# Kernel tuning notes

Hardware: AMD Instinct MI355X
Metric: run time of the kernel (lower is better)

Reference implementation:

```python
import jax, jax.numpy as jnp
import numpy as np

B, S, D = 4, 2048, 1024
H, HD = 16, 64  # n_heads, head_dim (n_kv_heads == n_heads -> n_rep = 1)
WINDOW = 256
ROPE_THETA = 10000.0


def setup_inputs() -> dict:
    key = jax.random.key(0)
    ks = jax.random.split(key, 5)
    x = jax.random.normal(ks[0], (B, S, D), dtype=jnp.float32)
    scale = 0.02
    wq = jax.random.normal(ks[1], (D, D), dtype=jnp.float32) * scale
    wk = jax.random.normal(ks[2], (D, D), dtype=jnp.float32) * scale
    wv = jax.random.normal(ks[3], (D, D), dtype=jnp.float32) * scale
    wo = jax.random.normal(ks[4], (D, D), dtype=jnp.float32) * scale
    # RoPE frequencies: freqs_cis[t, i] = exp(1j * t / theta^(2i/HD)), i in [0, HD/2)
    inv_freq = 1.0 / (ROPE_THETA ** (jnp.arange(0, HD, 2, dtype=jnp.float32) / HD))
    t = jnp.arange(S, dtype=jnp.float32)
    ang = t[:, None] * inv_freq[None, :]  # [S, HD/2]
    return {"x": x, "freqs_cos": jnp.cos(ang), "freqs_sin": jnp.sin(ang),
            "wq": wq, "wk": wk, "wv": wv, "wo": wo}


def _apply_rope(xq, xk, cos, sin):
    # xq/xk: [B, S, H, HD]; cos/sin: [S, HD/2] broadcast as [1, S, 1, HD/2]
    def rot(v):
        vr = v.reshape(*v.shape[:-1], HD // 2, 2)
        v0, v1 = vr[..., 0], vr[..., 1]
        c = cos[None, :, None, :]
        s = sin[None, :, None, :]
        o0 = v0 * c - v1 * s
        o1 = v0 * s + v1 * c
        return jnp.stack([o0, o1], axis=-1).reshape(v.shape)
    return rot(xq), rot(xk)


def reference(x, freqs_cos, freqs_sin, wq, wk, wv, wo):
    b, s, _ = x.shape
    xq = (x @ wq.T).reshape(b, s, H, HD)
    xk = (x @ wk.T).reshape(b, s, H, HD)
    xv = (x @ wv.T).reshape(b, s, H, HD)
    xq, xk = _apply_rope(xq, xk, freqs_cos, freqs_sin)
    # [B, H, S, S] scores
    scores = jnp.einsum('bqhd,bkhd->bhqk', xq, xk) / jnp.sqrt(jnp.float32(HD))
    pos = jnp.arange(s)
    # masked (disallowed) when j > i (future) or i - j >= window
    bad = (pos[None, :] > pos[:, None]) | (pos[:, None] - pos[None, :] >= WINDOW)
    scores = jnp.where(bad[None, None], -jnp.inf, scores)
    attn = jax.nn.softmax(scores.astype(jnp.float32), axis=-1).astype(xq.dtype)
    out = jnp.einsum('bhqk,bkhd->bqhd', attn, xv).reshape(b, s, H * HD)
    return out @ wo.T
```

## Files before the change

kernel.cpp:

```cpp
#include <hip/hip_runtime.h>
#include <hip/hip_bf16.h>


typedef __bf16 bf16_t;
typedef __attribute__((ext_vector_type(8))) __bf16 bf16x8;
typedef __attribute__((ext_vector_type(4))) __bf16 bf16x4;
typedef __attribute__((ext_vector_type(4))) float f32x4;

#define MFMA16(a, b, c) __builtin_amdgcn_mfma_f32_16x16x32_bf16((a), (b), (c), 0, 0, 0)

__device__ __forceinline__ void async16(const void* g, void* l) {
    __builtin_amdgcn_global_load_lds(
        (const __attribute__((address_space(1))) unsigned int*)g,
        (__attribute__((address_space(3))) unsigned int*)l, 16, 0, 0);
}

#define BAR() do { asm volatile("" ::: "memory"); __builtin_amdgcn_s_barrier(); \
                   asm volatile("" ::: "memory"); } while (0)
#define VMC(N) asm volatile("s_waitcnt vmcnt(" #N ")" ::: "memory")
#define LGKM0() asm volatile("s_waitcnt lgkmcnt(0)" ::: "memory")

#define CBS 131072L

__global__ __launch_bounds__(256) void cvt_all(const float* __restrict__ x,
                                               const float* __restrict__ wq,
                                               const float* __restrict__ wk,
                                               const float* __restrict__ wv,
                                               const float* __restrict__ wo,
                                               bf16_t* __restrict__ xbf,
                                               bf16_t* __restrict__ wqkv,
                                               bf16_t* __restrict__ wobf) {
    const int blk = blockIdx.x;
    const float* s;
    bf16_t* d;
    int base;
    if (blk < 4096)      { s = x;  d = xbf;            base = blk; }
    else if (blk < 4608) { s = wq; d = wqkv;           base = blk - 4096; }
    else if (blk < 5120) { s = wk; d = wqkv + 1048576; base = blk - 4608; }
    else if (blk < 5632) { s = wv; d = wqkv + 2097152; base = blk - 5120; }
    else                 { s = wo; d = wobf;           base = blk - 5632; }
    const int i = (base * 256 + threadIdx.x) * 8;
    float4 a = *(const float4*)(s + i);
    float4 b = *(const float4*)(s + i + 4);
    bf16x8 o;
    o[0] = (bf16_t)a.x; o[1] = (bf16_t)a.y; o[2] = (bf16_t)a.z; o[3] = (bf16_t)a.w;
    o[4] = (bf16_t)b.x; o[5] = (bf16_t)b.y; o[6] = (bf16_t)b.z; o[7] = (bf16_t)b.w;
    *(bf16x8*)(d + i) = o;
}

__global__ __launch_bounds__(512, 1) __attribute__((amdgpu_waves_per_eu(2)))
void gemm192_qkv(const bf16_t* __restrict__ A, const bf16_t* __restrict__ Bw,
                 const float* __restrict__ fcos, const float* __restrict__ fsin,
                 bf16_t* __restrict__ Qo, bf16_t* __restrict__ Ko,
                 bf16_t* __restrict__ VT, int M, int N, int K) {
    __shared__ __attribute__((aligned(16))) bf16_t As[32768];
    __shared__ __attribute__((aligned(16))) bf16_t Bs[24576];
    const int tid = threadIdx.x;
    const int l = tid & 63, w = tid >> 6;
    const int lr = l & 15, lg = l >> 4;
    const int wr = w >> 2, wc = w & 3;

    const int nwg = gridDim.x * gridDim.y;
    const int flat = blockIdx.y * gridDim.x + blockIdx.x;
    const int swz = (flat & 7) * (nwg >> 3) + (flat >> 3);
    const int bx = swz % gridDim.x, by = swz / gridDim.x;
    const long m0 = (long)by * 256, n0 = (long)bx * 192;
    const int NT = K >> 6;
    const int NI = NT >> 1;

    const int p  = w * 1024 + l * 16;
    const int pp = p ^ (((p >> 9) & 1) << 5);
    const int st = pp >> 10;
    const int rSt = (st >> 1) * 16 + ((pp >> 6) & 15);
    const int cSt = (st & 1) * 32 + ((pp >> 4) & 3) * 8;
    const bf16_t* aS = A  + (m0 + rSt) * K + cSt;
    const bf16_t* bS = Bw + (n0 + rSt) * K + cSt;
    const long uK = 64L * K;

    auto stageA = [&](int b, int u, int t) {
        async16(aS + (long)u * uK + (long)t * 64,
                (char*)As + b * 32768 + u * 8192 + w * 1024);
    };
    auto stageB = [&](int b, int u, int t) {
        async16(bS + (long)u * uK + (long)t * 64,
                (char*)Bs + b * 24576 + u * 8192 + w * 1024);
    };

    f32x4 acc[8][3] = {};
    bf16x8 afX[4], afY[4], bfX[3], bfY[3];
    const int swd = (lr & 8) << 2;

    auto loadAF = [&](int b, int mh, int ks, bf16x8 (&dst)[4]) {
#pragma unroll
        for (int mi = 0; mi < 4; ++mi) {
            const int off = (wr * 2 + mh) * 8192 + (mi * 2 + ks) * 1024 +
                            lr * 64 + lg * 16;
            dst[mi] = *(const bf16x8*)((const char*)As + b * 32768 + (off ^ swd));
        }
    };
    auto loadBF = [&](int b, int ks, bf16x8 (&dst)[3]) {
#pragma unroll
        for (int nj = 0; nj < 3; ++nj) {
            const int rg = wc * 48 + nj * 16 + lr;
            const int off = (rg >> 6) * 8192 + (((rg >> 4) & 3) * 2 + ks) * 1024 +
                            lr * 64 + lg * 16;
            dst[nj] = *(const bf16x8*)((const char*)Bs + b * 24576 + (off ^ swd));
        }
    };

#define QMM(MH, AF, BF) do {                                                   \
    __builtin_amdgcn_s_setprio(1);                                             \
    _Pragma("unroll")                                                          \
    for (int mi = 0; mi < 4; ++mi)                                             \
        _Pragma("unroll")                                                      \
        for (int nj = 0; nj < 3; ++nj)                                         \
            acc[(MH)*4+mi][nj] = MFMA16((AF)[mi], (BF)[nj], acc[(MH)*4+mi][nj]); \
    __builtin_amdgcn_s_setprio(0);                                             \
} while (0)

    stageA(0, 0, 0); stageA(0, 1, 0); stageA(0, 2, 0); stageA(0, 3, 0);
    stageB(0, 0, 0); stageB(0, 1, 0); stageB(0, 2, 0);
    stageB(1, 0, 1); stageB(1, 1, 1); stageB(1, 2, 1);
    VMC(3);
    BAR();

#pragma unroll 1
    for (int it = 0; it < NI - 1; ++it) {
        const int T = 2 * it;
        loadAF(0, 0, 0, afX); loadBF(0, 0, bfX);
        stageA(1, 0, T + 1); stageA(1, 1, T + 1);
        BAR(); QMM(0, afX, bfX); BAR();
        loadAF(0, 1, 0, afY);
        stageA(1, 2, T + 1); stageA(1, 3, T + 1);
        BAR(); QMM(1, afY, bfX); BAR();
        loadAF(0, 0, 1, afX); loadBF(0, 1, bfY);
        BAR(); QMM(0, afX, bfY); BAR();
        loadAF(0, 1, 1, afY);
        stageB(0, 0, T + 2);
        BAR(); QMM(1, afY, bfY); VMC(1); BAR();
        loadAF(1, 0, 0, afX); loadBF(1, 0, bfX);
        stageB(0, 1, T + 2); stageB(0, 2, T + 2);
        BAR(); QMM(0, afX, bfX); BAR();
        loadAF(1, 1, 0, afY);
        stageA(0, 0, T + 2); stageA(0, 1, T + 2);
        BAR(); QMM(1, afY, bfX); BAR();
        loadAF(1, 0, 1, afX); loadBF(1, 1, bfY);
        stageA(0, 2, T + 2); stageA(0, 3, T + 2);
        BAR(); QMM(0, afX, bfY); BAR();
        loadAF(1, 1, 1, afY);
        stageB(1, 0, T + 3); stageB(1, 1, T + 3); stageB(1, 2, T + 3);
        BAR(); QMM(1, afY, bfY); VMC(3); BAR();
    }

    {
        loadAF(0, 0, 0, afX); loadBF(0, 0, bfX);
        stageA(1, 0, NT - 1); stageA(1, 1, NT - 1);
        BAR(); QMM(0, afX, bfX); BAR();
        loadAF(0, 1, 0, afY);
        stageA(1, 2, NT - 1); stageA(1, 3, NT - 1);
        BAR(); QMM(1, afY, bfX); BAR();
        loadAF(0, 0, 1, afX); loadBF(0, 1, bfY);
        BAR(); QMM(0, afX, bfY); BAR();
        loadAF(0, 1, 1, afY);
        BAR(); QMM(1, afY, bfY);
        VMC(0); BAR();
        loadAF(1, 0, 0, afX); loadBF(1, 0, bfX);
        QMM(0, afX, bfX);
        loadAF(1, 1, 0, afY);
        QMM(1, afY, bfX);
        loadAF(1, 0, 1, afX); loadBF(1, 1, bfY);
        QMM(0, afX, bfY);
        loadAF(1, 1, 1, afY);
        QMM(1, afY, bfY);
    }
#undef QMM

    bf16_t* scr = (w < 6) ? (bf16_t*)((char*)As + w * 5120)
                          : (bf16_t*)((char*)Bs + (w - 6) * 5120);
    asm volatile("" ::: "memory");

    const int tl = l & 31, cg = l >> 5;
    const int chb = cg * 8;

#pragma unroll
    for (int nj = 0; nj < 3; ++nj) {
        const int cbase = (int)n0 + wc * 48 + nj * 16;
        const int cls = cbase >> 10;

#pragma unroll
        for (int ai = 0; ai < 8; ++ai)
#pragma unroll
            for (int j = 0; j < 4; ++j)
                scr[(ai * 16 + lg * 4 + j) * 20 + lr] = (bf16_t)acc[ai][nj][j];
        LGKM0();
        asm volatile("" ::: "memory");

        if (cls == 2) {
            const int ch = l >> 2;
            const int sub = l & 3;
            const int d16 = cbase - 2048 + ch;
            const int hh = d16 >> 6, dd = d16 & 63;
            const long T0 = m0 + wr * 128;
            const int bb = (int)(T0 >> 11);
            const int s0 = (int)(T0 & 2047);
            bf16_t* vrow = VT + ((long)((bb * 16 + hh) * 64 + dd) * 2048) + s0;
#pragma unroll
            for (int qq = 0; qq < 4; ++qq) {
                const int tb8 = qq * 32 + sub * 8;
                bf16x8 o;
#pragma unroll
                for (int j = 0; j < 8; ++j) {
                    const int f = ((j & 3) << 1) | (j >> 2);
                    o[j] = scr[(tb8 + f) * 20 + ch];
                }
                *(bf16x8*)(vrow + tb8) = o;
            }
        } else {
            const int cq = cbase & 1023;
            const float sc = (cls == 0) ? 0.125f : 1.f;
            bf16_t* qk = ((cls == 0) ? Qo : Ko) + (long)(cq >> 4) * CBS + chb;
            const int p2b = ((cbase & 63) >> 1) + cg * 4;
#pragma unroll
            for (int qq = 0; qq < 4; ++qq) {
                const int t = tl + qq * 32;
                bf16x4 vlo = *(const bf16x4*)&scr[t * 20 + chb];
                bf16x4 vhi = *(const bf16x4*)&scr[t * 20 + chb + 4];
                const long gt = m0 + wr * 128 + t;
                const int s0 = (int)(gt & 2047);
                const float4 cc = *(const float4*)(fcos + s0 * 32 + p2b);
                const float4 sn = *(const float4*)(fsin + s0 * 32 + p2b);
                bf16x8 o;
                float e0, e1;
                e0 = (float)vlo[0]; e1 = (float)vlo[1];
                o[0] = (bf16_t)((e0 * cc.x - e1 * sn.x) * sc);
                o[1] = (bf16_t)((e0 * sn.x + e1 * cc.x) * sc);
                e0 = (float)vlo[2]; e1 = (float)vlo[3];
                o[2] = (bf16_t)((e0 * cc.y - e1 * sn.y) * sc);
                o[3] = (bf16_t)((e0 * sn.y + e1 * cc.y) * sc);
                e0 = (float)vhi[0]; e1 = (float)vhi[1];
                o[4] = (bf16_t)((e0 * cc.z - e1 * sn.z) * sc);
                o[5] = (bf16_t)((e0 * sn.z + e1 * cc.z) * sc);
                e0 = (float)vhi[2]; e1 = (float)vhi[3];
                o[6] = (bf16_t)((e0 * cc.w - e1 * sn.w) * sc);
                o[7] = (bf16_t)((e0 * sn.w + e1 * cc.w) * sc);
                *(bf16x8*)(qk + gt * 16) = o;
            }
        }
        LGKM0();
        asm volatile("" ::: "memory");
    }
}

template <typename OUT>
__global__ __launch_bounds__(512, 2) void gemm256(const bf16_t* __restrict__ A,
                                                  const bf16_t* __restrict__ Bw,
                                                  OUT* __restrict__ C,
                                                  int M, int N, int K) {
    __shared__ __attribute__((aligned(16))) bf16_t As[49152];
    __shared__ __attribute__((aligned(16))) bf16_t Bs[24576];
    const int tid = threadIdx.x;
    const int l = tid & 63, w = tid >> 6;
    const int lr = l & 15, lg = l >> 4;
    const int wr = w >> 1, wc = w & 1;

    const int nwg = gridDim.x * gridDim.y;
    const int flat = blockIdx.y * gridDim.x + blockIdx.x;
    const int swz = (flat & 7) * (nwg >> 3) + (flat >> 3);
    const int bx = swz % gridDim.x, by = swz / gridDim.x;
    const long m0 = (long)by * 256, n0 = (long)bx * 128;
    const int NT = K >> 6;

    int rS[2], cS[2];
#pragma unroll
    for (int i = 0; i < 2; ++i) {
        const int p  = i * 8192 + w * 1024 + l * 16;
        const int pp = p ^ (((p >> 9) & 1) << 5);
        const int st = pp >> 10;
        rS[i] = (st >> 1) * 16 + ((pp >> 6) & 15);
        cS[i] = (st & 1) * 32 + ((pp >> 4) & 3) * 8;
    }
    const bf16_t* aSrc0 = A  + (m0 + rS[0]) * K + cS[0];
    const bf16_t* aSrc1 = A  + (m0 + rS[1]) * K + cS[1];
    const bf16_t* bSrc0 = Bw + (n0 + rS[0]) * K + cS[0];
    const bf16_t* bSrc1 = Bw + (n0 + rS[1]) * K + cS[1];
    const long hK = 128L * K;

    auto stageA = [&](int b, int h, int t) {
        char* d = (char*)As + b * 32768 + h * 16384 + w * 1024;
        const long o = (long)h * hK + (long)t * 64;
        async16(aSrc0 + o, d);
        async16(aSrc1 + o, d + 8192);
    };
    auto stageB = [&](int b, int t) {
        char* d = (char*)Bs + b * 16384 + w * 1024;
        const long o = (long)t * 64;
        async16(bSrc0 + o, d);
        async16(bSrc1 + o, d + 8192);
    };

    f32x4 acc[4][4] = {};
    bf16x8 af[4][2], blo[2][2], bhi[2][2];
    const int swd = (lr & 8) << 2;

    auto loadA = [&](int b) {
#pragma unroll
        for (int mi = 0; mi < 4; ++mi)
#pragma unroll
            for (int ks = 0; ks < 2; ++ks) {
                const int ra = (wr & 1) * 64 + mi * 16 + lr;
                const int off = ((ra >> 4) * 2 + ks) * 1024 + (ra & 15) * 64 + lg * 16;
                af[mi][ks] = *(const bf16x8*)((const char*)As + b * 32768 +
                                              (wr >> 1) * 16384 + (off ^ swd));
            }
    };
    auto loadB = [&](int b, int nh, bf16x8 (&dst)[2][2]) {
#pragma unroll
        for (int nj = 0; nj < 2; ++nj)
#pragma unroll
            for (int ks = 0; ks < 2; ++ks) {
                const int rb = wc * 64 + (nh * 2 + nj) * 16 + lr;
                const int off = ((rb >> 4) * 2 + ks) * 1024 + (rb & 15) * 64 + lg * 16;
                dst[nj][ks] = *(const bf16x8*)((const char*)Bs + b * 16384 +
                                               (off ^ swd));
            }
    };

#define QMM(NH, BF) do {                                                       \
    __builtin_amdgcn_s_setprio(1);                                             \
    _Pragma("unroll")                                                          \
    for (int mi = 0; mi < 4; ++mi) {                                           \
        acc[mi][(NH)*2]   = MFMA16(af[mi][0], (BF)[0][0], acc[mi][(NH)*2]);    \
        acc[mi][(NH)*2]   = MFMA16(af[mi][1], (BF)[0][1], acc[mi][(NH)*2]);    \
        acc[mi][(NH)*2+1] = MFMA16(af[mi][0], (BF)[1][0], acc[mi][(NH)*2+1]);  \
        acc[mi][(NH)*2+1] = MFMA16(af[mi][1], (BF)[1][1], acc[mi][(NH)*2+1]);  \
    }                                                                          \
    __builtin_amdgcn_s_setprio(0);                                             \
} while (0)

    stageA(0, 0, 0); stageA(0, 1, 0); stageB(0, 0);
    stageA(1, 0, 1); stageA(1, 1, 1); stageB(1, 1);
    VMC(6);
    BAR();

    int bc = 0;
#pragma unroll 1
    for (int t = 0; t < NT - 2; ++t) {
        const int bn = (bc + 2 >= 3) ? bc - 1 : bc + 2;
        loadA(bc); loadB(bc, 0, blo); stageA(bn, 0, t + 2); stageA(bn, 1, t + 2);
        BAR(); QMM(0, blo); BAR();
        loadB(bc, 1, bhi); stageB(bn, t + 2);
        BAR(); QMM(1, bhi);
        if (t < NT - 3) { VMC(6); } else { VMC(0); }
        BAR();
        bc = (bc + 1 >= 3) ? 0 : bc + 1;
    }
    {
        loadA(bc); loadB(bc, 0, blo);
        QMM(0, blo);
        loadB(bc, 1, bhi);
        QMM(1, bhi);
        const int b2 = (bc + 1 >= 3) ? 0 : bc + 1;
        loadA(b2); loadB(b2, 0, blo);
        QMM(0, blo);
        loadB(b2, 1, bhi);
        QMM(1, bhi);
    }
#undef QMM

#pragma unroll
    for (int mi = 0; mi < 4; ++mi)
#pragma unroll
        for (int ni = 0; ni < 4; ++ni)
#pragma unroll
            for (int j = 0; j < 4; ++j) {
                long r = m0 + wr * 64 + mi * 16 + lg * 4 + j;
                long c = n0 + wc * 64 + ni * 16 + lr;
                C[r * N + c] = (OUT)acc[mi][ni][j];
            }
}

__global__ __launch_bounds__(256, 4) void attn_win4(const bf16_t* __restrict__ Q,
                                                    const bf16_t* __restrict__ Kb,
                                                    const bf16_t* __restrict__ VT,
                                                    bf16_t* __restrict__ Ao) {
    __shared__ __attribute__((aligned(16))) bf16_t kld[2 * 4096];
    __shared__ __attribute__((aligned(16))) bf16_t vld[2 * 4096];
    const int raw = blockIdx.x;
    const int mswz = ((raw & 7) << 8) | (raw >> 3);
    const int qt = mswz & 31, bh = mswz >> 5;
    const int h = bh & 15, b = bh >> 4;
    const int l = threadIdx.x & 63, w = threadIdx.x >> 6;
    const int lr = l & 15, lg = l >> 4;
    const int q0 = qt * 64 + w * 16;
    const int q = q0 + lr;
    const int tb = qt - 4;

    const bf16_t* Qh = Q  + (long)(4 * h) * CBS + (long)(b * 2048) * 16;
    const bf16_t* Kh = Kb + (long)(4 * h) * CBS + (long)(b * 2048) * 16;
    const bf16_t* Vp = VT + (long)bh * 64 * 2048;

    auto stageT = [&](int u, int bs) {
        const int kt = tb + u;
        const int kt64 = (kt < 0 ? 0 : kt) * 64;
#pragma unroll
        for (int part = 0; part < 2; ++part) {
            const int seg = w * 2 + part;
            const int r = seg * 8 + (l >> 3);
            const int sc = (l & 7) ^ ((r >> 1) & 7);
            async16(Kh + (sc >> 1) * CBS + (long)(kt64 + r) * 16 + (sc & 1) * 8,
                    (char*)kld + bs * 8192 + seg * 1024);
            async16(Vp + (long)r * 2048 + kt64 + sc * 8,
                    (char*)vld + bs * 8192 + seg * 1024);
        }
    };

    stageT(0, 0);
    const bf16x8 qb0 = *(const bf16x8*)&Qh[(lg >> 1) * CBS + (long)q * 16 + (lg & 1) * 8];
    const bf16x8 qb1 = *(const bf16x8*)&Qh[(2 + (lg >> 1)) * CBS + (long)q * 16 + (lg & 1) * 8];
    VMC(0);
    BAR();

    float mrun = -1000.f, lsum = 0.f;
    f32x4 o0 = {0.f, 0.f, 0.f, 0.f}, o1 = {0.f, 0.f, 0.f, 0.f};
    f32x4 o2 = {0.f, 0.f, 0.f, 0.f}, o3 = {0.f, 0.f, 0.f, 0.f};
    const int swv = (lr >> 1) & 7;

    const char* kbase;
    const char* vbase;
    int k0s;

#define QKCORE(HH, MM)                                                           \
        const int row_ = (HH) * 32 + 2 * lr + (MM);                              \
        const int sw_ = (row_ >> 1) & 7;                                         \
        bf16x8 k0_ = *(const bf16x8*)(kbase + row_ * 128 + ((lg ^ sw_) << 4));   \
        bf16x8 k1_ = *(const bf16x8*)(kbase + row_ * 128 + (((4 + lg) ^ sw_) << 4)); \
        f32x4 s_ = {0.f, 0.f, 0.f, 0.f};                                         \
        s_ = MFMA16(k0_, qb0, s_);                                               \
        s_ = MFMA16(k1_, qb1, s_);

#define QKF_F(DST, HH, MM)                                                       \
    f32x4 DST; { QKCORE(HH, MM)                                                  \
        const int kb_ = k0s + (HH) * 32 + (MM) + lg * 8;                         \
        DST[0] = ((kb_ >= 0) & ((unsigned)(q - kb_) < 256u))         ? s_[0] : -1e30f; \
        DST[1] = ((kb_ + 2 >= 0) & ((unsigned)(q - kb_ - 2) < 256u)) ? s_[1] : -1e30f; \
        DST[2] = ((kb_ + 4 >= 0) & ((unsigned)(q - kb_ - 4) < 256u)) ? s_[2] : -1e30f; \
        DST[3] = ((kb_ + 6 >= 0) & ((unsigned)(q - kb_ - 6) < 256u)) ? s_[3] : -1e30f; \
    }

#define QKF_U(DST, HH, MM)                                                       \
    f32x4 DST; { QKCORE(HH, MM)                                                  \
        const int d_ = q - (k0s + (HH) * 32 + (MM) + lg * 8);                    \
        DST[0] = (d_ < 256)     ? s_[0] : -1e30f;                                \
        DST[1] = (d_ - 2 < 256) ? s_[1] : -1e30f;                                \
        DST[2] = (d_ - 4 < 256) ? s_[2] : -1e30f;                                \
        DST[3] = (d_ - 6 < 256) ? s_[3] : -1e30f;                                \
    }

#define QKF_L(DST, HH, MM)                                                       \
    f32x4 DST; { QKCORE(HH, MM)                                                  \
        const int d_ = q - (k0s + (HH) * 32 + (MM) + lg * 8);                    \
        DST[0] = (d_ >= 0)     ? s_[0] : -1e30f;                                 \
        DST[1] = (d_ - 2 >= 0) ? s_[1] : -1e30f;                                 \
        DST[2] = (d_ - 4 >= 0) ? s_[2] : -1e30f;                                 \
        DST[3] = (d_ - 6 >= 0) ? s_[3] : -1e30f;                                 \
    }

#define QKF_N(DST, HH, MM)                                                       \
    f32x4 DST; { QKCORE(HH, MM)                                                  \
        DST[0] = s_[0]; DST[1] = s_[1]; DST[2] = s_[2]; DST[3] = s_[3];          \
    }

#define EXV(S_) {                                                                \
        S_[0] = __expf(S_[0] - mnew); S_[1] = __expf(S_[1] - mnew);              \
        S_[2] = __expf(S_[2] - mnew); S_[3] = __expf(S_[3] - mnew);              \
        rs += (S_[0] + S_[1]) + (S_[2] + S_[3]); }

#define PVF(NT, HH, PB) {                                                        \
        bf16x8 va_ = *(const bf16x8*)(vbase + ((NT) * 16 + lr) * 128 +           \
                                      ((((HH) * 4 + lg) ^ swv) << 4));           \
        o##NT = MFMA16(va_, PB, o##NT); }

#define TILEBODY(QKM) {                                                          \
        QKM(sA, 0, 0) QKM(sB, 0, 1) QKM(sC, 1, 0) QKM(sD, 1, 1)                  \
        float tm = fmaxf(fmaxf(fmaxf(sA[0], sA[1]), fmaxf(sA[2], sA[3])),        \
                         fmaxf(fmaxf(sB[0], sB[1]), fmaxf(sB[2], sB[3])));       \
        tm = fmaxf(tm, fmaxf(fmaxf(fmaxf(sC[0], sC[1]), fmaxf(sC[2], sC[3])),    \
                             fmaxf(fmaxf(sD[0], sD[1]), fmaxf(sD[2], sD[3]))));  \
        tm = fmaxf(tm, __shfl_xor(tm, 16));                                      \
        tm = fmaxf(tm, __shfl_xor(tm, 32));                                      \
        const float mnew = fmaxf(mrun, tm);                                      \
        const float alpha = __expf(mrun - mnew);                                 \
        mrun = mnew;                                                             \
        float rs = 0.f;                                                          \
        EXV(sA) EXV(sB) EXV(sC) EXV(sD)                                          \
        rs += __shfl_xor(rs, 16);                                                \
        rs += __shfl_xor(rs, 32);                                                \
        lsum = lsum * alpha + rs;                                                \
        o0[0] *= alpha; o0[1] *= alpha; o0[2] *= alpha; o0[3] *= alpha;          \
        o1[0] *= alpha; o1[1] *= alpha; o1[2] *= alpha; o1[3] *= alpha;          \
        o2[0] *= alpha; o2[1] *= alpha; o2[2] *= alpha; o2[3] *= alpha;          \
        o3[0] *= alpha; o3[1] *= alpha; o3[2] *= alpha; o3[3] *= alpha;          \
        bf16x8 pb0, pb1;                                                         \
        pb0[0] = (bf16_t)sA[0]; pb0[1] = (bf16_t)sA[1]; pb0[2] = (bf16_t)sA[2]; pb0[3] = (bf16_t)sA[3]; \
        pb0[4] = (bf16_t)sB[0]; pb0[5] = (bf16_t)sB[1]; pb0[6] = (bf16_t)sB[2]; pb0[7] = (bf16_t)sB[3]; \
        pb1[0] = (bf16_t)sC[0]; pb1[1] = (bf16_t)sC[1]; pb1[2] = (bf16_t)sC[2]; pb1[3] = (bf16_t)sC[3]; \
        pb1[4] = (bf16_t)sD[0]; pb1[5] = (bf16_t)sD[1]; pb1[6] = (bf16_t)sD[2]; pb1[7] = (bf16_t)sD[3]; \
        PVF(0, 0, pb0) PVF(1, 0, pb0) PVF(2, 0, pb0) PVF(3, 0, pb0)              \
        PVF(0, 1, pb1) PVF(1, 1, pb1) PVF(2, 1, pb1) PVF(3, 1, pb1)              \
    }

#define ITER(U, QKM) {                                                           \
        if ((U) < 4) stageT((U) + 1, ((U) + 1) & 1);                             \
        kbase = (const char*)kld + ((U) & 1) * 8192;                             \
        vbase = (const char*)vld + ((U) & 1) * 8192;                             \
        k0s = (tb + (U)) * 64;                                                   \
        TILEBODY(QKM)                                                            \
        if ((U) < 4) { VMC(0); BAR(); }                                          \
    }

    if (qt >= 4) {
        ITER(0, QKF_U)
        ITER(1, QKF_N)
        ITER(2, QKF_N)
        ITER(3, QKF_N)
        ITER(4, QKF_L)
    } else {
        ITER(0, QKF_F)
        ITER(1, QKF_F)
        ITER(2, QKF_F)
        ITER(3, QKF_F)
        ITER(4, QKF_F)
    }
#undef ITER
#undef TILEBODY
#undef QKF_F
#undef QKF_U
#undef QKF_L
#undef QKF_N
#undef QKCORE
#undef EXV
#undef PVF

    const float rinv = 1.0f / lsum;
    bf16_t* aor = Ao + ((long)(b * 2048) + q) * 1024 + h * 64;
#define EPI(NT, OA_) {                                                           \
        bf16x4 ov_;                                                             \
        ov_[0] = (bf16_t)(OA_[0] * rinv); ov_[1] = (bf16_t)(OA_[1] * rinv);      \
        ov_[2] = (bf16_t)(OA_[2] * rinv); ov_[3] = (bf16_t)(OA_[3] * rinv);      \
        *(bf16x4*)(aor + (NT) * 16 + lg * 4) = ov_; }
    EPI(0, o0) EPI(1, o1) EPI(2, o2) EPI(3, o3)
#undef EPI
}

extern "C" void kernel_launch(void* const* d_in, const int* in_sizes, int n_in,
                              void* d_out, int out_size, void* d_ws, size_t ws_size,
                              hipStream_t stream) {
    (void)in_sizes; (void)n_in; (void)out_size; (void)ws_size;
    const float* x    = (const float*)d_in[0];
    const float* fcos = (const float*)d_in[1];
    const float* fsin = (const float*)d_in[2];
    const float* wq   = (const float*)d_in[3];
    const float* wk   = (const float*)d_in[4];
    const float* wv   = (const float*)d_in[5];
    const float* wo   = (const float*)d_in[6];
    float* out = (float*)d_out;

    char* ws = (char*)d_ws;
    bf16_t* xbf   = (bf16_t*)(ws);
    bf16_t* wqkv  = (bf16_t*)(ws + 16777216);
    bf16_t* wobf  = (bf16_t*)(ws + 23068672);
    bf16_t* qbuf  = (bf16_t*)(ws + 41943040);
    bf16_t* kbuf  = (bf16_t*)(ws + 75497472);
    bf16_t* vtb   = (bf16_t*)(ws + 92274688);
    bf16_t* aob   = xbf;

    cvt_all<<<6144, 256, 0, stream>>>(x, wq, wk, wv, wo, xbf, wqkv, wobf);

    gemm192_qkv<<<dim3(16, 32), 512, 0, stream>>>(xbf, wqkv, fcos, fsin,
                                                  qbuf, kbuf, vtb,
                                                  8192, 3072, 1024);
    attn_win4<<<2048, 256, 0, stream>>>(qbuf, kbuf, vtb, aob);
    gemm256<float><<<dim3(8, 32), 512, 0, stream>>>(aob, wobf, out, 8192, 1024, 1024);
}
```

Baseline: 120.6 us.

## Widen QKV GEMM tile from 256x192 to 256x256 with restructured pipeline

The QKV projection GEMM now uses 256x256 output tiles instead of 256x192, so the grid shrinks from 16x32 to 12x32 workgroups. Each wave now computes a 128x64 block with 8x4 accumulators. Staging and fragment loads are reorganised into half-tiles with a new barrier and wait schedule. The goal is higher arithmetic intensity and less redundant A-operand traffic. The cost is more registers, more LDS, and 384 workgroups, which is fewer than the 512 before and may leave the GPU's CUs less evenly loaded.

```diff
diff --git a/kernel.cpp b/kernel.cpp
--- a/kernel.cpp
+++ b/kernel.cpp
@@ -49,12 +49,12 @@
 }
 
 __global__ __launch_bounds__(512, 1) __attribute__((amdgpu_waves_per_eu(2)))
-void gemm192_qkv(const bf16_t* __restrict__ A, const bf16_t* __restrict__ Bw,
+void gemm256_qkv(const bf16_t* __restrict__ A, const bf16_t* __restrict__ Bw,
                  const float* __restrict__ fcos, const float* __restrict__ fsin,
                  bf16_t* __restrict__ Qo, bf16_t* __restrict__ Ko,
                  bf16_t* __restrict__ VT, int M, int N, int K) {
     __shared__ __attribute__((aligned(16))) bf16_t As[32768];
-    __shared__ __attribute__((aligned(16))) bf16_t Bs[24576];
+    __shared__ __attribute__((aligned(16))) bf16_t Bs[32768];
     const int tid = threadIdx.x;
     const int l = tid & 63, w = tid >> 6;
     const int lr = l & 15, lg = l >> 4;
@@ -64,114 +64,118 @@
     const int flat = blockIdx.y * gridDim.x + blockIdx.x;
     const int swz = (flat & 7) * (nwg >> 3) + (flat >> 3);
     const int bx = swz % gridDim.x, by = swz / gridDim.x;
-    const long m0 = (long)by * 256, n0 = (long)bx * 192;
+    const long m0 = (long)by * 256, n0 = (long)bx * 256;
     const int NT = K >> 6;
     const int NI = NT >> 1;
 
-    const int p  = w * 1024 + l * 16;
-    const int pp = p ^ (((p >> 9) & 1) << 5);
-    const int st = pp >> 10;
-    const int rSt = (st >> 1) * 16 + ((pp >> 6) & 15);
-    const int cSt = (st & 1) * 32 + ((pp >> 4) & 3) * 8;
-    const bf16_t* aS = A  + (m0 + rSt) * K + cSt;
-    const bf16_t* bS = Bw + (n0 + rSt) * K + cSt;
-    const long uK = 64L * K;
-
-    auto stageA = [&](int b, int u, int t) {
-        async16(aS + (long)u * uK + (long)t * 64,
-                (char*)As + b * 32768 + u * 8192 + w * 1024);
-    };
-    auto stageB = [&](int b, int u, int t) {
-        async16(bS + (long)u * uK + (long)t * 64,
-                (char*)Bs + b * 24576 + u * 8192 + w * 1024);
-    };
-
-    f32x4 acc[8][3] = {};
-    bf16x8 afX[4], afY[4], bfX[3], bfY[3];
+    int rS[2], cS[2];
+#pragma unroll
+    for (int i = 0; i < 2; ++i) {
+        const int p  = i * 8192 + w * 1024 + l * 16;
+        const int pp = p ^ (((p >> 9) & 1) << 5);
+        const int st = pp >> 10;
+        rS[i] = (st >> 1) * 16 + ((pp >> 6) & 15);
+        cS[i] = (st & 1) * 32 + ((pp >> 4) & 3) * 8;
+    }
+    const bf16_t* aSrc0 = A  + (m0 + rS[0]) * K + cS[0];
+    const bf16_t* aSrc1 = A  + (m0 + rS[1]) * K + cS[1];
+    const bf16_t* bSrc0 = Bw + (n0 + rS[0]) * K + cS[0];
+    const bf16_t* bSrc1 = Bw + (n0 + rS[1]) * K + cS[1];
+    const long hK = 128L * K;
+
+    auto stageA = [&](int b, int h, int t) {
+        char* d = (char*)As + b * 32768 + h * 16384 + w * 1024;
+        const long o = (long)h * hK + (long)t * 64;
+        async16(aSrc0 + o, d);
+        async16(aSrc1 + o, d + 8192);
+    };
+    auto stageB = [&](int b, int h, int t) {
+        char* d = (char*)Bs + b * 32768 + h * 16384 + w * 1024;
+        const long o = (long)h * hK + (long)t * 64;
+        async16(bSrc0 + o, d);
+        async16(bSrc1 + o, d + 8192);
+    };
+
+    f32x4 acc[8][4] = {};
+    bf16x8 af[4][2], bh0[2][2], bh1[2][2];
     const int swd = (lr & 8) << 2;
 
-    auto loadAF = [&](int b, int mh, int ks, bf16x8 (&dst)[4]) {
-#pragma unroll
-        for (int mi = 0; mi < 4; ++mi) {
-            const int off = (wr * 2 + mh) * 8192 + (mi * 2 + ks) * 1024 +
-                            lr * 64 + lg * 16;
-            dst[mi] = *(const bf16x8*)((const char*)As + b * 32768 + (off ^ swd));
-        }
-    };
-    auto loadBF = [&](int b, int ks, bf16x8 (&dst)[3]) {
-#pragma unroll
-        for (int nj = 0; nj < 3; ++nj) {
-            const int rg = wc * 48 + nj * 16 + lr;
-            const int off = (rg >> 6) * 8192 + (((rg >> 4) & 3) * 2 + ks) * 1024 +
-                            lr * 64 + lg * 16;
-            dst[nj] = *(const bf16x8*)((const char*)Bs + b * 24576 + (off ^ swd));
-        }
-    };
-
-#define QMM(MH, AF, BF) do {                                                   \
-    __builtin_amdgcn_s_setprio(1);                                             \
-    _Pragma("unroll")                                                          \
-    for (int mi = 0; mi < 4; ++mi)                                             \
-        _Pragma("unroll")                                                      \
-        for (int nj = 0; nj < 3; ++nj)                                         \
-            acc[(MH)*4+mi][nj] = MFMA16((AF)[mi], (BF)[nj], acc[(MH)*4+mi][nj]); \
-    __builtin_amdgcn_s_setprio(0);                                             \
+    auto loadA = [&](int b, int mh) {
+#pragma unroll
+        for (int i = 0; i < 4; ++i)
+#pragma unroll
+            for (int ks = 0; ks < 2; ++ks) {
+                const int off = ((mh * 4 + i) * 2 + ks) * 1024 + lr * 64 + lg * 16;
+                af[i][ks] = *(const bf16x8*)((const char*)As + b * 32768 +
+                                             wr * 16384 + (off ^ swd));
+            }
+    };
+    auto loadB = [&](int b, int nh, bf16x8 (&dst)[2][2]) {
+#pragma unroll
+        for (int j = 0; j < 2; ++j)
+#pragma unroll
+            for (int ks = 0; ks < 2; ++ks) {
+                const int off = (((wc & 1) * 4 + nh * 2 + j) * 2 + ks) * 1024 +
+                                lr * 64 + lg * 16;
+                dst[j][ks] = *(const bf16x8*)((const char*)Bs + b * 32768 +
+                                              (wc >> 1) * 16384 + (off ^ swd));
+            }
+    };
+
+#define QMM(MH, NH, BF) do {                                                        \
+    __builtin_amdgcn_s_setprio(1);                                                  \
+    _Pragma("unroll")                                                               \
+    for (int qi = 0; qi < 4; ++qi) {                                                \
+        acc[(MH)*4+qi][(NH)*2]   = MFMA16(af[qi][0], (BF)[0][0], acc[(MH)*4+qi][(NH)*2]);   \
+        acc[(MH)*4+qi][(NH)*2]   = MFMA16(af[qi][1], (BF)[0][1], acc[(MH)*4+qi][(NH)*2]);   \
+        acc[(MH)*4+qi][(NH)*2+1] = MFMA16(af[qi][0], (BF)[1][0], acc[(MH)*4+qi][(NH)*2+1]); \
+        acc[(MH)*4+qi][(NH)*2+1] = MFMA16(af[qi][1], (BF)[1][1], acc[(MH)*4+qi][(NH)*2+1]); \
+    }                                                                               \
+    __builtin_amdgcn_s_setprio(0);                                                  \
 } while (0)
 
-    stageA(0, 0, 0); stageA(0, 1, 0); stageA(0, 2, 0); stageA(0, 3, 0);
-    stageB(0, 0, 0); stageB(0, 1, 0); stageB(0, 2, 0);
-    stageB(1, 0, 1); stageB(1, 1, 1); stageB(1, 2, 1);
-    VMC(3);
+    stageB(0, 0, 0); stageB(0, 1, 0); stageA(0, 0, 0); stageA(0, 1, 0);
+    stageB(1, 0, 1); stageB(1, 1, 1);
+    VMC(4);
     BAR();
 
 #pragma unroll 1
     for (int it = 0; it < NI - 1; ++it) {
-        const int T = 2 * it;
-        loadAF(0, 0, 0, afX); loadBF(0, 0, bfX);
-        stageA(1, 0, T + 1); stageA(1, 1, T + 1);
-        BAR(); QMM(0, afX, bfX); BAR();
-        loadAF(0, 1, 0, afY);
-        stageA(1, 2, T + 1); stageA(1, 3, T + 1);
-        BAR(); QMM(1, afY, bfX); BAR();
-        loadAF(0, 0, 1, afX); loadBF(0, 1, bfY);
-        BAR(); QMM(0, afX, bfY); BAR();
-        loadAF(0, 1, 1, afY);
-        stageB(0, 0, T + 2);
-        BAR(); QMM(1, afY, bfY); VMC(1); BAR();
-        loadAF(1, 0, 0, afX); loadBF(1, 0, bfX);
-        stageB(0, 1, T + 2); stageB(0, 2, T + 2);
-        BAR(); QMM(0, afX, bfX); BAR();
-        loadAF(1, 1, 0, afY);
-        stageA(0, 0, T + 2); stageA(0, 1, T + 2);
-        BAR(); QMM(1, afY, bfX); BAR();
-        loadAF(1, 0, 1, afX); loadBF(1, 1, bfY);
-        stageA(0, 2, T + 2); stageA(0, 3, T + 2);
-        BAR(); QMM(0, afX, bfY); BAR();
-        loadAF(1, 1, 1, afY);
-        stageB(1, 0, T + 3); stageB(1, 1, T + 3); stageB(1, 2, T + 3);
-        BAR(); QMM(1, afY, bfY); VMC(3); BAR();
+        const int T = it * 2;
+        loadA(0, 0); loadB(0, 0, bh0); stageA(1, 0, T + 1);
+        BAR(); QMM(0, 0, bh0); BAR();
+        loadB(0, 1, bh1); stageA(1, 1, T + 1);
+        BAR(); QMM(0, 1, bh1); BAR();
+        loadA(0, 1); stageB(0, 0, T + 2);
+        BAR(); QMM(1, 0, bh0); BAR();
+        stageB(0, 1, T + 2);
+        BAR(); QMM(1, 1, bh1); VMC(4); BAR();
+        loadA(1, 0); loadB(1, 0, bh0); stageA(0, 0, T + 2);
+        BAR(); QMM(0, 0, bh0); BAR();
+        loadB(1, 1, bh1); stageA(0, 1, T + 2);
+        BAR(); QMM(0, 1, bh1); BAR();
+        loadA(1, 1); stageB(1, 0, T + 3);
+        BAR(); QMM(1, 0, bh0); BAR();
+        stageB(1, 1, T + 3);
+        BAR(); QMM(1, 1, bh1); VMC(4); BAR();
     }
 
     {
-        loadAF(0, 0, 0, afX); loadBF(0, 0, bfX);
-        stageA(1, 0, NT - 1); stageA(1, 1, NT - 1);
-        BAR(); QMM(0, afX, bfX); BAR();
-        loadAF(0, 1, 0, afY);
-        stageA(1, 2, NT - 1); stageA(1, 3, NT - 1);
-        BAR(); QMM(1, afY, bfX); BAR();
-        loadAF(0, 0, 1, afX); loadBF(0, 1, bfY);
-        BAR(); QMM(0, afX, bfY); BAR();
-        loadAF(0, 1, 1, afY);
-        BAR(); QMM(1, afY, bfY);
+        const int T = NT - 2;
+        loadA(0, 0); loadB(0, 0, bh0); stageA(1, 0, T + 1);
+        BAR(); QMM(0, 0, bh0); BAR();
+        loadB(0, 1, bh1); stageA(1, 1, T + 1);
+        BAR(); QMM(0, 1, bh1); BAR();
+        loadA(0, 1);
+        BAR(); QMM(1, 0, bh0); QMM(1, 1, bh1);
         VMC(0); BAR();
-        loadAF(1, 0, 0, afX); loadBF(1, 0, bfX);
-        QMM(0, afX, bfX);
-        loadAF(1, 1, 0, afY);
-        QMM(1, afY, bfX);
-        loadAF(1, 0, 1, afX); loadBF(1, 1, bfY);
-        QMM(0, afX, bfY);
-        loadAF(1, 1, 1, afY);
-        QMM(1, afY, bfY);
+        loadA(1, 0); loadB(1, 0, bh0);
+        QMM(0, 0, bh0);
+        loadB(1, 1, bh1);
+        QMM(0, 1, bh1);
+        loadA(1, 1);
+        QMM(1, 0, bh0);
+        QMM(1, 1, bh1);
     }
 #undef QMM
 
@@ -183,15 +187,15 @@
     const int chb = cg * 8;
 
 #pragma unroll
-    for (int nj = 0; nj < 3; ++nj) {
-        const int cbase = (int)n0 + wc * 48 + nj * 16;
+    for (int ni = 0; ni < 4; ++ni) {
+        const int cbase = (int)n0 + wc * 64 + ni * 16;
         const int cls = cbase >> 10;
 
 #pragma unroll
         for (int ai = 0; ai < 8; ++ai)
 #pragma unroll
             for (int j = 0; j < 4; ++j)
-                scr[(ai * 16 + lg * 4 + j) * 20 + lr] = (bf16_t)acc[ai][nj][j];
+                scr[(ai * 16 + lg * 4 + j) * 20 + lr] = (bf16_t)acc[ai][ni][j];
         LGKM0();
         asm volatile("" ::: "memory");
 
@@ -576,7 +580,7 @@
 
     cvt_all<<<6144, 256, 0, stream>>>(x, wq, wk, wv, wo, xbf, wqkv, wobf);
 
-    gemm192_qkv<<<dim3(16, 32), 512, 0, stream>>>(xbf, wqkv, fcos, fsin,
+    gemm256_qkv<<<dim3(12, 32), 512, 0, stream>>>(xbf, wqkv, fcos, fsin,
                                                   qbuf, kbuf, vtb,
                                                   8192, 3072, 1024);
     attn_win4<<<2048, 256, 0, stream>>>(qbuf, kbuf, vtb, aob);
```

New measurement: 138.1 us. +14.5%, slower.

## Restructure output-projection GEMM with double-buffered LDS and 2x4 wave layout

Applied to the files above, without the earlier changes.

Replaces the triple-buffered output projection GEMM with a double-buffered version that uses less LDS. The 8 waves are rearranged into a 2x4 grid, each computing 128x32, and loads and MFMAs are interleaved at finer granularity with per-quarter staging and barriers. The aim is to raise occupancy (waves_per_eu 2) and overlap global-to-LDS copies with compute better. In exchange it adds more barriers and has a shallower prefetch depth, which may expose memory latency.

```diff
diff --git a/kernel.cpp b/kernel.cpp
--- a/kernel.cpp
+++ b/kernel.cpp
@@ -251,17 +251,15 @@
     }
 }
 
-template <typename OUT>
-__global__ __launch_bounds__(512, 2) void gemm256(const bf16_t* __restrict__ A,
-                                                  const bf16_t* __restrict__ Bw,
-                                                  OUT* __restrict__ C,
-                                                  int M, int N, int K) {
-    __shared__ __attribute__((aligned(16))) bf16_t As[49152];
-    __shared__ __attribute__((aligned(16))) bf16_t Bs[24576];
+__global__ __launch_bounds__(512, 1) __attribute__((amdgpu_waves_per_eu(2)))
+void gemm128_o(const bf16_t* __restrict__ A, const bf16_t* __restrict__ Bw,
+               float* __restrict__ C, int M, int N, int K) {
+    __shared__ __attribute__((aligned(16))) bf16_t As[32768];
+    __shared__ __attribute__((aligned(16))) bf16_t Bs[16384];
     const int tid = threadIdx.x;
     const int l = tid & 63, w = tid >> 6;
     const int lr = l & 15, lg = l >> 4;
-    const int wr = w >> 1, wc = w & 1;
+    const int wr = w >> 2, wc = w & 3;
 
     const int nwg = gridDim.x * gridDim.y;
     const int flat = blockIdx.y * gridDim.x + blockIdx.x;
@@ -269,113 +267,123 @@
     const int bx = swz % gridDim.x, by = swz / gridDim.x;
     const long m0 = (long)by * 256, n0 = (long)bx * 128;
     const int NT = K >> 6;
-
-    int rS[2], cS[2];
-#pragma unroll
-    for (int i = 0; i < 2; ++i) {
-        const int p  = i * 8192 + w * 1024 + l * 16;
-        const int pp = p ^ (((p >> 9) & 1) << 5);
-        const int st = pp >> 10;
-        rS[i] = (st >> 1) * 16 + ((pp >> 6) & 15);
-        cS[i] = (st & 1) * 32 + ((pp >> 4) & 3) * 8;
-    }
-    const bf16_t* aSrc0 = A  + (m0 + rS[0]) * K + cS[0];
-    const bf16_t* aSrc1 = A  + (m0 + rS[1]) * K + cS[1];
-    const bf16_t* bSrc0 = Bw + (n0 + rS[0]) * K + cS[0];
-    const bf16_t* bSrc1 = Bw + (n0 + rS[1]) * K + cS[1];
-    const long hK = 128L * K;
-
-    auto stageA = [&](int b, int h, int t) {
-        char* d = (char*)As + b * 32768 + h * 16384 + w * 1024;
-        const long o = (long)h * hK + (long)t * 64;
-        async16(aSrc0 + o, d);
-        async16(aSrc1 + o, d + 8192);
-    };
-    auto stageB = [&](int b, int t) {
-        char* d = (char*)Bs + b * 16384 + w * 1024;
-        const long o = (long)t * 64;
-        async16(bSrc0 + o, d);
-        async16(bSrc1 + o, d + 8192);
-    };
-
-    f32x4 acc[4][4] = {};
-    bf16x8 af[4][2], blo[2][2], bhi[2][2];
+    const int NI = NT >> 1;
+
+    const int p  = w * 1024 + l * 16;
+    const int pp = p ^ (((p >> 9) & 1) << 5);
+    const int st = pp >> 10;
+    const int rSt = (st >> 1) * 16 + ((pp >> 6) & 15);
+    const int cSt = (st & 1) * 32 + ((pp >> 4) & 3) * 8;
+    const bf16_t* aS = A  + (m0 + rSt) * K + cSt;
+    const bf16_t* bS = Bw + (n0 + rSt) * K + cSt;
+    const long uK = 64L * K;
+
+    auto stageA = [&](int b, int u, int t) {
+        async16(aS + (long)u * uK + (long)t * 64,
+                (char*)As + b * 32768 + u * 8192 + w * 1024);
+    };
+    auto stageB = [&](int b, int u, int t) {
+        async16(bS + (long)u * uK + (long)t * 64,
+                (char*)Bs + b * 16384 + u * 8192 + w * 1024);
+    };
+
+    f32x4 acc[8][2] = {};
+    bf16x8 afX[4], afY[4], bfX[2], bfY[2];
     const int swd = (lr & 8) << 2;
 
-    auto loadA = [&](int b) {
-#pragma unroll
-        for (int mi = 0; mi < 4; ++mi)
-#pragma unroll
-            for (int ks = 0; ks < 2; ++ks) {
-                const int ra = (wr & 1) * 64 + mi * 16 + lr;
-                const int off = ((ra >> 4) * 2 + ks) * 1024 + (ra & 15) * 64 + lg * 16;
-                af[mi][ks] = *(const bf16x8*)((const char*)As + b * 32768 +
-                                              (wr >> 1) * 16384 + (off ^ swd));
-            }
-    };
-    auto loadB = [&](int b, int nh, bf16x8 (&dst)[2][2]) {
-#pragma unroll
-        for (int nj = 0; nj < 2; ++nj)
-#pragma unroll
-            for (int ks = 0; ks < 2; ++ks) {
-                const int rb = wc * 64 + (nh * 2 + nj) * 16 + lr;
-                const int off = ((rb >> 4) * 2 + ks) * 1024 + (rb & 15) * 64 + lg * 16;
-                dst[nj][ks] = *(const bf16x8*)((const char*)Bs + b * 16384 +
-                                               (off ^ swd));
-            }
-    };
-
-#define QMM(NH, BF) do {                                                       \
+    auto loadAF = [&](int b, int mh, int ks, bf16x8 (&dst)[4]) {
+#pragma unroll
+        for (int mi = 0; mi < 4; ++mi) {
+            const int off = (wr * 2 + mh) * 8192 + (mi * 2 + ks) * 1024 +
+                            lr * 64 + lg * 16;
+            dst[mi] = *(const bf16x8*)((const char*)As + b * 32768 + (off ^ swd));
+        }
+    };
+    auto loadBF = [&](int b, int ks, bf16x8 (&dst)[2]) {
+#pragma unroll
+        for (int nj = 0; nj < 2; ++nj) {
+            const int rg = wc * 32 + nj * 16 + lr;
+            const int off = (rg >> 6) * 8192 + (((rg >> 4) & 3) * 2 + ks) * 1024 +
+                            lr * 64 + lg * 16;
+            dst[nj] = *(const bf16x8*)((const char*)Bs + b * 16384 + (off ^ swd));
+        }
+    };
+
+#define QMM(MH, AF, BF) do {                                                   \
     __builtin_amdgcn_s_setprio(1);                                             \
     _Pragma("unroll")                                                          \
-    for (int mi = 0; mi < 4; ++mi) {                                           \
-        acc[mi][(NH)*2]   = MFMA16(af[mi][0], (BF)[0][0], acc[mi][(NH)*2]);    \
-        acc[mi][(NH)*2]   = MFMA16(af[mi][1], (BF)[0][1], acc[mi][(NH)*2]);    \
-        acc[mi][(NH)*2+1] = MFMA16(af[mi][0], (BF)[1][0], acc[mi][(NH)*2+1]);  \
-        acc[mi][(NH)*2+1] = MFMA16(af[mi][1], (BF)[1][1], acc[mi][(NH)*2+1]);  \
-    }                                                                          \
+    for (int mi = 0; mi < 4; ++mi)                                             \
+        _Pragma("unroll")                                                      \
+        for (int nj = 0; nj < 2; ++nj)                                         \
+            acc[(MH)*4+mi][nj] = MFMA16((AF)[mi], (BF)[nj], acc[(MH)*4+mi][nj]); \
     __builtin_amdgcn_s_setprio(0);                                             \
 } while (0)
 
-    stageA(0, 0, 0); stageA(0, 1, 0); stageB(0, 0);
-    stageA(1, 0, 1); stageA(1, 1, 1); stageB(1, 1);
-    VMC(6);
+    stageA(0, 0, 0); stageA(0, 1, 0); stageA(0, 2, 0); stageA(0, 3, 0);
+    stageB(0, 0, 0); stageB(0, 1, 0);
+    stageB(1, 0, 1); stageB(1, 1, 1);
+    VMC(2);
     BAR();
 
-    int bc = 0;
 #pragma unroll 1
-    for (int t = 0; t < NT - 2; ++t) {
-        const int bn = (bc + 2 >= 3) ? bc - 1 : bc + 2;
-        loadA(bc); loadB(bc, 0, blo); stageA(bn, 0, t + 2); stageA(bn, 1, t + 2);
-        BAR(); QMM(0, blo); BAR();
-        loadB(bc, 1, bhi); stageB(bn, t + 2);
-        BAR(); QMM(1, bhi);
-        if (t < NT - 3) { VMC(6); } else { VMC(0); }
-        BAR();
-        bc = (bc + 1 >= 3) ? 0 : bc + 1;
-    }
+    for (int it = 0; it < NI - 1; ++it) {
+        const int T = 2 * it;
+        loadAF(0, 0, 0, afX); loadBF(0, 0, bfX);
+        stageA(1, 0, T + 1); stageA(1, 1, T + 1);
+        BAR(); QMM(0, afX, bfX); BAR();
+        loadAF(0, 1, 0, afY);
+        stageA(1, 2, T + 1); stageA(1, 3, T + 1);
+        BAR(); QMM(1, afY, bfX); BAR();
+        loadAF(0, 0, 1, afX); loadBF(0, 1, bfY);
+        BAR(); QMM(0, afX, bfY); BAR();
+        loadAF(0, 1, 1, afY);
+        stageB(0, 0, T + 2); stageB(0, 1, T + 2);
+        BAR(); QMM(1, afY, bfY); VMC(2); BAR();
+        loadAF(1, 0, 0, afX); loadBF(1, 0, bfX);
+        stageA(0, 0, T + 2); stageA(0, 1, T + 2);
+        BAR(); QMM(0, afX, bfX); BAR();
+        loadAF(1, 1, 0, afY);
+        stageA(0, 2, T + 2); stageA(0, 3, T + 2);
+        BAR(); QMM(1, afY, bfX); BAR();
+        loadAF(1, 0, 1, afX); loadBF(1, 1, bfY);
+        BAR(); QMM(0, afX, bfY); BAR();
+        loadAF(1, 1, 1, afY);
+        stageB(1, 0, T + 3); stageB(1, 1, T + 3);
+        BAR(); QMM(1, afY, bfY); VMC(2); BAR();
+    }
+
     {
-        loadA(bc); loadB(bc, 0, blo);
-        QMM(0, blo);
-        loadB(bc, 1, bhi);
-        QMM(1, bhi);
-        const int b2 = (bc + 1 >= 3) ? 0 : bc + 1;
-        loadA(b2); loadB(b2, 0, blo);
-        QMM(0, blo);
-        loadB(b2, 1, bhi);
-        QMM(1, bhi);
+        loadAF(0, 0, 0, afX); loadBF(0, 0, bfX);
+        stageA(1, 0, NT - 1); stageA(1, 1, NT - 1);
+        BAR(); QMM(0, afX, bfX); BAR();
+        loadAF(0, 1, 0, afY);
+        stageA(1, 2, NT - 1); stageA(1, 3, NT - 1);
+        BAR(); QMM(1, afY, bfX); BAR();
+        loadAF(0, 0, 1, afX); loadBF(0, 1, bfY);
+        BAR(); QMM(0, afX, bfY); BAR();
+        loadAF(0, 1, 1, afY);
+        BAR(); QMM(1, afY, bfY);
+        VMC(0); BAR();
+        loadAF(1, 0, 0, afX); loadBF(1, 0, bfX);
+        QMM(0, afX, bfX);
+        loadAF(1, 1, 0, afY);
+        QMM(1, afY, bfX);
+        loadAF(1, 0, 1, afX); loadBF(1, 1, bfY);
+        QMM(0, afX, bfY);
+        loadAF(1, 1, 1, afY);
+        QMM(1, afY, bfY);
     }
 #undef QMM
 
 #pragma unroll
-    for (int mi = 0; mi < 4; ++mi)
-#pragma unroll
-        for (int ni = 0; ni < 4; ++ni)
+    for (int ai = 0; ai < 8; ++ai)
+#pragma unroll
+        for (int nj = 0; nj < 2; ++nj)
 #pragma unroll
             for (int j = 0; j < 4; ++j) {
-                long r = m0 + wr * 64 + mi * 16 + lg * 4 + j;
-                long c = n0 + wc * 64 + ni * 16 + lr;
-                C[r * N + c] = (OUT)acc[mi][ni][j];
+                long r = m0 + wr * 128 + ai * 16 + lg * 4 + j;
+                long c = n0 + wc * 32 + nj * 16 + lr;
+                C[r * (long)N + c] = acc[ai][nj][j];
             }
 }
 
@@ -580,5 +588,5 @@
                                                   qbuf, kbuf, vtb,
                                                   8192, 3072, 1024);
     attn_win4<<<2048, 256, 0, stream>>>(qbuf, kbuf, vtb, aob);
-    gemm256<float><<<dim3(8, 32), 512, 0, stream>>>(aob, wobf, out, 8192, 1024, 1024);
+    gemm128_o<<<dim3(8, 32), 512, 0, stream>>>(aob, wobf, out, 8192, 1024, 1024);
 }
```

Result: no change. 122.7 us (+1.8%).
